# Performance work log

Measured on AMD Instinct MI355X. Metric: run time of the kernel, lower is better.

The kernel has to match this reference:

```python
import jax, jax.numpy as jnp
import numpy as np

N = 50000      # nodes
E = 1600000    # edges (avg degree 32)
IN = 128       # input feature dim
H = 4          # heads
C = 16         # out channels per head
NEG_SLOPE = 0.2


def setup_inputs() -> dict:
    key = jax.random.key(0)
    k = jax.random.split(key, 6)
    x = jax.random.normal(k[0], (N, IN), jnp.float32)
    edge_index = jax.random.randint(k[1], (2, E), 0, N, dtype=jnp.int32).astype(jnp.int64)
    W = jax.random.normal(k[2], (H * C, IN), jnp.float32) * (1.0 / np.sqrt(IN))
    att_src = jax.random.normal(k[3], (H, C), jnp.float32) * 0.1
    att_dst = jax.random.normal(k[4], (H, C), jnp.float32) * 0.1
    bias = jax.random.normal(k[5], (H * C,), jnp.float32) * 0.01
    return {"x": x, "edge_index": edge_index, "W": W,
            "att_src": att_src, "att_dst": att_dst, "bias": bias}


def reference(x, edge_index, W, att_src, att_dst, bias):
    # shared linear projection (PyG GATConv lin, no bias): [N, H, C]
    xp = (x @ W.T).reshape(-1, H, C)
    # per-node attention logits: [N, H]
    a_src = jnp.einsum('nhc,hc->nh', xp, att_src)
    a_dst = jnp.einsum('nhc,hc->nh', xp, att_dst)
    src, dst = edge_index[0], edge_index[1]  # messages flow src(j) -> dst(i)
    # per-edge scores: [E, H]
    e = jax.nn.leaky_relu(a_src[src] + a_dst[dst], negative_slope=NEG_SLOPE)
    # segment softmax over destination neighborhoods
    m = jax.ops.segment_max(e, dst, num_segments=N)           # [N, H]
    m = jnp.where(jnp.isfinite(m), m, 0.0)                     # empty segments
    ex = jnp.exp(e - m[dst])
    s = jax.ops.segment_sum(ex, dst, num_segments=N)           # [N, H]
    alpha = ex / (s[dst] + 1e-16)                              # [E, H]
    # weighted messages, scatter-add to destinations
    msg = (alpha[:, :, None] * xp[src]).reshape(E, H * C)      # [E, H*C]
    out = jax.ops.segment_sum(msg, dst, num_segments=N)        # [N, H*C]
    return out + bias
```

## Files before the change

### kernel.cpp

```cpp
#include <hip/hip_runtime.h>
#include <hip/hip_bf16.h>
#include <math.h>

#define N_NODES 50000
#define N_EDGES 1600000
#define IN_DIM  128
#define HC      64
#define NH      4
#define SLOTS   72
#define BSHIFT  6
#define BNODES  64
#define NB      782
#define BCAP    2432
#define BIN_BLOCKS 250
#define BIN_G   1600
#define GEMM_BLOCKS 391
#define GEMM_LDS 33792

__global__ __launch_bounds__(512) void bin_count_kernel(
    const int* __restrict__ ei, int* __restrict__ counts) {
    __shared__ int lcount[NB];
    int tid = (int)threadIdx.x;
    int bx  = (int)blockIdx.x;
    for (int j = tid; j < NB; j += 512) lcount[j] = 0;
    __syncthreads();
    const int4* dp = (const int4*)(ei + N_EDGES);
    int g0 = bx * BIN_G;
#pragma unroll
    for (int it = 0; it < 4; ++it) {
        int gi = it * 512 + tid;
        if (gi < BIN_G) {
            int4 dv = dp[g0 + gi];
            atomicAdd(&lcount[dv.x >> BSHIFT], 1);
            atomicAdd(&lcount[dv.y >> BSHIFT], 1);
            atomicAdd(&lcount[dv.z >> BSHIFT], 1);
            atomicAdd(&lcount[dv.w >> BSHIFT], 1);
        }
    }
    __syncthreads();
    for (int j = tid; j < NB; j += 512)
        counts[bx * NB + j] = lcount[j];
}

__global__ __launch_bounds__(256) void bin_scan_kernel(
    const int* __restrict__ counts, int* __restrict__ base,
    int* __restrict__ btot) {
    __shared__ int sc[256];
    int j = (int)blockIdx.x, t = (int)threadIdx.x;
    int v = (t < BIN_BLOCKS) ? counts[t * NB + j] : 0;
    sc[t] = v;
    __syncthreads();
#pragma unroll
    for (int off = 1; off < 256; off <<= 1) {
        int u = (t >= off) ? sc[t - off] : 0;
        __syncthreads();
        sc[t] += u;
        __syncthreads();
    }
    if (t < BIN_BLOCKS) base[t * NB + j] = sc[t] - v;
    if (t == BIN_BLOCKS - 1) btot[j] = sc[t];
}

__global__ __launch_bounds__(512) void bin_append_kernel(
    const int* __restrict__ ei, const int* __restrict__ base,
    unsigned int* __restrict__ barr) {
    __shared__ int lbase[NB], lcnt[NB];
    int tid = (int)threadIdx.x;
    int bx  = (int)blockIdx.x;
    for (int j = tid; j < NB; j += 512) {
        lbase[j] = base[bx * NB + j];
        lcnt[j]  = 0;
    }
    __syncthreads();
    const int4* sp = (const int4*)ei;
    const int4* dp = (const int4*)(ei + N_EDGES);
    int g0 = bx * BIN_G;
#pragma unroll
    for (int it = 0; it < 4; ++it) {
        int gi = it * 512 + tid;
        if (gi < BIN_G) {
            int4 sv = sp[g0 + gi];
            int4 dv = dp[g0 + gi];
            int s[4] = {sv.x, sv.y, sv.z, sv.w};
            int d[4] = {dv.x, dv.y, dv.z, dv.w};
#pragma unroll
            for (int u = 0; u < 4; ++u) {
                int bk = d[u] >> BSHIFT;
                int lp = atomicAdd(&lcnt[bk], 1);
                int pos = lbase[bk] + lp;
                if (pos < BCAP)
                    barr[(size_t)bk * BCAP + pos] =
                        (unsigned)s[u] | ((unsigned)(d[u] & (BNODES - 1)) << 20);
            }
        }
    }
}

__global__ __launch_bounds__(512) void gemm_kernel(
    const float* __restrict__ x, const float* __restrict__ W,
    const float* __restrict__ att_src, const float* __restrict__ att_dst,
    __hip_bfloat16* __restrict__ xp, float* __restrict__ a_src,
    float* __restrict__ a_dst) {
    extern __shared__ char smraw[];
    int tid = (int)threadIdx.x;
    int gb  = (int)blockIdx.x;
    float* Wl = (float*)smraw;
    const float4* W4 = (const float4*)W;
#pragma unroll
    for (int j = 0; j < 4; ++j) {
        int f = j * 512 + tid;
        int c = f >> 5, k4 = f & 31;
        *(float4*)&Wl[c * 132 + k4 * 4] = W4[f];
    }
    __syncthreads();

    int l = tid & 63, w = tid >> 6, q = l >> 4, i = l & 15;
    int n0 = gb * 128 + w * 16 + q * 4;
    int nj[4];
#pragma unroll
    for (int j = 0; j < 4; ++j) {
        int n = n0 + j;
        nj[j] = (n < N_NODES) ? n : N_NODES - 1;
    }
    const float* wlp = Wl + i * 132;
    float4 acc[4] = {{0,0,0,0},{0,0,0,0},{0,0,0,0},{0,0,0,0}};
    float4 xr[4], xn[4];
#pragma unroll
    for (int j = 0; j < 4; ++j) xr[j] = *(const float4*)(x + (size_t)nj[j] * IN_DIM);
#pragma unroll 2
    for (int k0 = 0; k0 < IN_DIM; k0 += 4) {
        if (k0 + 4 < IN_DIM) {
#pragma unroll
            for (int j = 0; j < 4; ++j)
                xn[j] = *(const float4*)(x + (size_t)nj[j] * IN_DIM + k0 + 4);
        }
        float4 wl0 = *(const float4*)(wlp + 0 * 16 * 132 + k0);
        float4 wl1 = *(const float4*)(wlp + 1 * 16 * 132 + k0);
        float4 wl2 = *(const float4*)(wlp + 2 * 16 * 132 + k0);
        float4 wl3 = *(const float4*)(wlp + 3 * 16 * 132 + k0);
#pragma unroll
        for (int j = 0; j < 4; ++j) {
            float4 xv = xr[j];
            acc[j].x = fmaf(xv.x, wl0.x, fmaf(xv.y, wl0.y, fmaf(xv.z, wl0.z, fmaf(xv.w, wl0.w, acc[j].x))));
            acc[j].y = fmaf(xv.x, wl1.x, fmaf(xv.y, wl1.y, fmaf(xv.z, wl1.z, fmaf(xv.w, wl1.w, acc[j].y))));
            acc[j].z = fmaf(xv.x, wl2.x, fmaf(xv.y, wl2.y, fmaf(xv.z, wl2.z, fmaf(xv.w, wl2.w, acc[j].z))));
            acc[j].w = fmaf(xv.x, wl3.x, fmaf(xv.y, wl3.y, fmaf(xv.z, wl3.z, fmaf(xv.w, wl3.w, acc[j].w))));
        }
#pragma unroll
        for (int j = 0; j < 4; ++j) xr[j] = xn[j];
    }

    float a_s0 = att_src[i], a_s1 = att_src[16 + i], a_s2 = att_src[32 + i], a_s3 = att_src[48 + i];
    float a_d0 = att_dst[i], a_d1 = att_dst[16 + i], a_d2 = att_dst[32 + i], a_d3 = att_dst[48 + i];
#pragma unroll
    for (int j = 0; j < 4; ++j) {
        int n = n0 + j;
        if (n < N_NODES) {
            __hip_bfloat16* xw = xp + (size_t)n * HC;
            xw[i]      = __float2bfloat16(acc[j].x);
            xw[16 + i] = __float2bfloat16(acc[j].y);
            xw[32 + i] = __float2bfloat16(acc[j].z);
            xw[48 + i] = __float2bfloat16(acc[j].w);
            float4 ps, pd;
            ps.x = acc[j].x * a_s0; ps.y = acc[j].y * a_s1;
            ps.z = acc[j].z * a_s2; ps.w = acc[j].w * a_s3;
            pd.x = acc[j].x * a_d0; pd.y = acc[j].y * a_d1;
            pd.z = acc[j].z * a_d2; pd.w = acc[j].w * a_d3;
#pragma unroll
            for (int off = 1; off < 16; off <<= 1) {
                ps.x += __shfl_xor(ps.x, off, 64); ps.y += __shfl_xor(ps.y, off, 64);
                ps.z += __shfl_xor(ps.z, off, 64); ps.w += __shfl_xor(ps.w, off, 64);
                pd.x += __shfl_xor(pd.x, off, 64); pd.y += __shfl_xor(pd.y, off, 64);
                pd.z += __shfl_xor(pd.z, off, 64); pd.w += __shfl_xor(pd.w, off, 64);
            }
            if (i == 0) {
                *(float4*)(a_src + n * NH) = ps;
                *(float4*)(a_dst + n * NH) = pd;
            }
        }
    }
}

__global__ __launch_bounds__(512) void fused_gather_kernel(
    const unsigned int* __restrict__ barr, const int* __restrict__ btot,
    const float* __restrict__ a_src, const float* __restrict__ a_dst,
    const __hip_bfloat16* __restrict__ xp, const float* __restrict__ bias,
    float* __restrict__ out) {
    __shared__ int lcsr[BNODES * SLOTS];
    __shared__ int deg[BNODES];
    int b = blockIdx.x, tid = (int)threadIdx.x;
    if (tid < BNODES) deg[tid] = 0;
    __syncthreads();
    int n = btot[b];
    n = (n < BCAP) ? n : BCAP;
    const unsigned int* src = barr + (size_t)b * BCAP;

    for (int i0 = 0; i0 < n; i0 += 2048) {
        int ibase = i0 + tid * 4;
        unsigned v[4]; bool val[4]; int dp[4], pos[4];
        if (ibase < n) {
            uint4 r = *(const uint4*)(src + ibase);
            v[0] = r.x; v[1] = r.y; v[2] = r.z; v[3] = r.w;
        } else { v[0] = v[1] = v[2] = v[3] = 0u; }
#pragma unroll
        for (int u = 0; u < 4; ++u) {
            val[u] = (ibase + u) < n;
            dp[u] = (int)(v[u] >> 20);
            if (val[u]) pos[u] = atomicAdd(&deg[dp[u]], 1);
        }
#pragma unroll
        for (int u = 0; u < 4; ++u)
            if (val[u] && pos[u] < SLOTS)
                lcsr[dp[u] * SLOTS + pos[u]] = (int)(v[u] & 0xFFFFF);
    }
    __syncthreads();

    int l = tid & 63;
    int w = tid >> 6;
    int g = l >> 3;
    int i = l & 7;
    int h = i >> 1;
    int dl = w * 8 + g;
    int dst = (b << BSHIFT) + dl;
    int dg = deg[dl];
    dg = (dg < SLOTS) ? dg : SLOTS;
    int dstc = (dst < N_NODES) ? dst : 0;
    float adh = a_dst[dstc * NH + h];

    int sreg[9];
#pragma unroll
    for (int k = 0; k < 9; ++k) sreg[k] = lcsr[dl * SLOTS + k * 8 + i];

    const unsigned short* xpi = (const unsigned short*)xp + 8 * i;
    const float* asrch = a_src + h;
    int gsel = l & 56;
    float a0=0,a1=0,a2=0,a3=0,a4=0,a5=0,a6=0,a7=0;
    float dsum = 0.f;

#pragma unroll
    for (int k = 0; k < 9; ++k) {
        if (dg > k * 8) {
            int cnt = dg - k * 8;
            int reg = sreg[k];
            int s8[8]; float g8[8]; uint4 t8[8];
#pragma unroll
            for (int u = 0; u < 8; ++u) {
                int raw = __shfl(reg, gsel | u, 64);
                s8[u] = (u < cnt) ? raw : 0;
            }
#pragma unroll
            for (int u = 0; u < 8; ++u) g8[u] = asrch[s8[u] * NH];
#pragma unroll
            for (int u = 0; u < 8; ++u)
                t8[u] = *(const uint4*)(xpi + (size_t)s8[u] * HC);
#pragma unroll
            for (int u = 0; u < 8; ++u) {
                float e = g8[u] + adh;
                e = fmaxf(e, 0.2f * e);
                float wv = (u < cnt) ? __expf(e) : 0.f;
                dsum += wv;
                uint4 t = t8[u];
                a0 = fmaf(wv, __uint_as_float(t.x << 16),          a0);
                a1 = fmaf(wv, __uint_as_float(t.x & 0xffff0000u),  a1);
                a2 = fmaf(wv, __uint_as_float(t.y << 16),          a2);
                a3 = fmaf(wv, __uint_as_float(t.y & 0xffff0000u),  a3);
                a4 = fmaf(wv, __uint_as_float(t.z << 16),          a4);
                a5 = fmaf(wv, __uint_as_float(t.z & 0xffff0000u),  a5);
                a6 = fmaf(wv, __uint_as_float(t.w << 16),          a6);
                a7 = fmaf(wv, __uint_as_float(t.w & 0xffff0000u),  a7);
            }
        }
    }
    if (dst < N_NODES) {
        float inv = 1.f / (dsum + 1e-16f);
        float4 b0 = *(const float4*)(bias + 8 * i);
        float4 b1 = *(const float4*)(bias + 8 * i + 4);
        float4 o0, o1;
        o0.x = a0 * inv + b0.x; o0.y = a1 * inv + b0.y;
        o0.z = a2 * inv + b0.z; o0.w = a3 * inv + b0.w;
        o1.x = a4 * inv + b1.x; o1.y = a5 * inv + b1.y;
        o1.z = a6 * inv + b1.z; o1.w = a7 * inv + b1.w;
        float* op = out + (size_t)dst * HC + 8 * i;
        *(float4*)op = o0;
        *(float4*)(op + 4) = o1;
    }
}

extern "C" void kernel_launch(void* const* d_in, const int* in_sizes, int n_in,
                              void* d_out, int out_size, void* d_ws, size_t ws_size,
                              hipStream_t stream) {
    const float* x       = (const float*)d_in[0];
    const int*   ei      = (const int*)d_in[1];
    const float* W       = (const float*)d_in[2];
    const float* att_src = (const float*)d_in[3];
    const float* att_dst = (const float*)d_in[4];
    const float* bias    = (const float*)d_in[5];
    float* out = (float*)d_out;

    char* ws = (char*)d_ws;
    __hip_bfloat16* xp      = (__hip_bfloat16*)(ws);
    float*          a_srcv  = (float*)(ws + 6400000);
    float*          a_dstv  = (float*)(ws + 7200000);
    int*            btot    = (int*)  (ws + 8000000);
    unsigned int*   barr    = (unsigned int*)(ws + 8016384);
    int*            counts  = (int*)  (ws + 15624192);
    int*            basem   = (int*)  (ws + 16406272);

    bin_count_kernel<<<BIN_BLOCKS, 512, 0, stream>>>(ei, counts);
    bin_scan_kernel<<<NB, 256, 0, stream>>>(counts, basem, btot);
    bin_append_kernel<<<BIN_BLOCKS, 512, 0, stream>>>(ei, basem, barr);
    gemm_kernel<<<GEMM_BLOCKS, 512, GEMM_LDS, stream>>>(
        x, W, att_src, att_dst, xp, a_srcv, a_dstv);
    fused_gather_kernel<<<NB, 512, 0, stream>>>(barr, btot,
                                                a_srcv, a_dstv, xp, bias, out);
}
```

Baseline: 153.2 us.

## Fuse GEMM with bin counting, split bins finer, prefetch next gather group

Merges the projection GEMM and the edge bin-count pass into one launch. Extra blocks do the per-block destination histogram, so counting runs alongside the GEMM and one kernel launch disappears. Doubles the number of binning blocks (halving edges per block) and widens the scan to 512 threads to match. In the gather kernel, the shuffle of the next group's source indices and its a_src loads are issued before the current group's exp/FMA work, hiding that latency. The cost is more partial-count rows to scan and higher register pressure in the gather loop.

```diff
diff --git a/kernel.cpp b/kernel.cpp
--- a/kernel.cpp
+++ b/kernel.cpp
@@ -12,98 +12,47 @@
 #define BNODES  64
 #define NB      782
 #define BCAP    2432
-#define BIN_BLOCKS 250
-#define BIN_G   1600
+#define BIN_BLOCKS 500
+#define BIN_G   800
 #define GEMM_BLOCKS 391
+#define FAT_GRID (GEMM_BLOCKS + BIN_BLOCKS)
 #define GEMM_LDS 33792
 
-__global__ __launch_bounds__(512) void bin_count_kernel(
-    const int* __restrict__ ei, int* __restrict__ counts) {
-    __shared__ int lcount[NB];
+__global__ __launch_bounds__(512) void gemm_count_kernel(
+    const float* __restrict__ x, const float* __restrict__ W,
+    const float* __restrict__ att_src, const float* __restrict__ att_dst,
+    const int* __restrict__ ei,
+    __hip_bfloat16* __restrict__ xp, float* __restrict__ a_src,
+    float* __restrict__ a_dst, int* __restrict__ counts) {
+    extern __shared__ char smraw[];
     int tid = (int)threadIdx.x;
     int bx  = (int)blockIdx.x;
-    for (int j = tid; j < NB; j += 512) lcount[j] = 0;
-    __syncthreads();
-    const int4* dp = (const int4*)(ei + N_EDGES);
-    int g0 = bx * BIN_G;
-#pragma unroll
-    for (int it = 0; it < 4; ++it) {
-        int gi = it * 512 + tid;
-        if (gi < BIN_G) {
-            int4 dv = dp[g0 + gi];
-            atomicAdd(&lcount[dv.x >> BSHIFT], 1);
-            atomicAdd(&lcount[dv.y >> BSHIFT], 1);
-            atomicAdd(&lcount[dv.z >> BSHIFT], 1);
-            atomicAdd(&lcount[dv.w >> BSHIFT], 1);
-        }
-    }
-    __syncthreads();
-    for (int j = tid; j < NB; j += 512)
-        counts[bx * NB + j] = lcount[j];
-}
-
-__global__ __launch_bounds__(256) void bin_scan_kernel(
-    const int* __restrict__ counts, int* __restrict__ base,
-    int* __restrict__ btot) {
-    __shared__ int sc[256];
-    int j = (int)blockIdx.x, t = (int)threadIdx.x;
-    int v = (t < BIN_BLOCKS) ? counts[t * NB + j] : 0;
-    sc[t] = v;
-    __syncthreads();
-#pragma unroll
-    for (int off = 1; off < 256; off <<= 1) {
-        int u = (t >= off) ? sc[t - off] : 0;
+
+    if (bx >= GEMM_BLOCKS) {
+        int cb = bx - GEMM_BLOCKS;
+        int* lcount = (int*)smraw;
+        for (int j = tid; j < NB; j += 512) lcount[j] = 0;
         __syncthreads();
-        sc[t] += u;
+        const int4* dp = (const int4*)(ei + N_EDGES);
+        int g0 = cb * BIN_G;
+#pragma unroll
+        for (int it = 0; it < 2; ++it) {
+            int gi = it * 512 + tid;
+            if (gi < BIN_G) {
+                int4 dv = dp[g0 + gi];
+                atomicAdd(&lcount[dv.x >> BSHIFT], 1);
+                atomicAdd(&lcount[dv.y >> BSHIFT], 1);
+                atomicAdd(&lcount[dv.z >> BSHIFT], 1);
+                atomicAdd(&lcount[dv.w >> BSHIFT], 1);
+            }
+        }
         __syncthreads();
-    }
-    if (t < BIN_BLOCKS) base[t * NB + j] = sc[t] - v;
-    if (t == BIN_BLOCKS - 1) btot[j] = sc[t];
-}
-
-__global__ __launch_bounds__(512) void bin_append_kernel(
-    const int* __restrict__ ei, const int* __restrict__ base,
-    unsigned int* __restrict__ barr) {
-    __shared__ int lbase[NB], lcnt[NB];
-    int tid = (int)threadIdx.x;
-    int bx  = (int)blockIdx.x;
-    for (int j = tid; j < NB; j += 512) {
-        lbase[j] = base[bx * NB + j];
-        lcnt[j]  = 0;
-    }
-    __syncthreads();
-    const int4* sp = (const int4*)ei;
-    const int4* dp = (const int4*)(ei + N_EDGES);
-    int g0 = bx * BIN_G;
-#pragma unroll
-    for (int it = 0; it < 4; ++it) {
-        int gi = it * 512 + tid;
-        if (gi < BIN_G) {
-            int4 sv = sp[g0 + gi];
-            int4 dv = dp[g0 + gi];
-            int s[4] = {sv.x, sv.y, sv.z, sv.w};
-            int d[4] = {dv.x, dv.y, dv.z, dv.w};
-#pragma unroll
-            for (int u = 0; u < 4; ++u) {
-                int bk = d[u] >> BSHIFT;
-                int lp = atomicAdd(&lcnt[bk], 1);
-                int pos = lbase[bk] + lp;
-                if (pos < BCAP)
-                    barr[(size_t)bk * BCAP + pos] =
-                        (unsigned)s[u] | ((unsigned)(d[u] & (BNODES - 1)) << 20);
-            }
-        }
-    }
-}
-
-__global__ __launch_bounds__(512) void gemm_kernel(
-    const float* __restrict__ x, const float* __restrict__ W,
-    const float* __restrict__ att_src, const float* __restrict__ att_dst,
-    __hip_bfloat16* __restrict__ xp, float* __restrict__ a_src,
-    float* __restrict__ a_dst) {
-    extern __shared__ char smraw[];
-    int tid = (int)threadIdx.x;
-    int gb  = (int)blockIdx.x;
+        for (int j = tid; j < NB; j += 512)
+            counts[cb * NB + j] = lcount[j];
+        return;
+    }
+
+    int gb = bx;
     float* Wl = (float*)smraw;
     const float4* W4 = (const float4*)W;
 #pragma unroll
@@ -181,6 +130,60 @@
     }
 }
 
+__global__ __launch_bounds__(512) void bin_scan_kernel(
+    const int* __restrict__ counts, int* __restrict__ base,
+    int* __restrict__ btot) {
+    __shared__ int sc[512];
+    int j = (int)blockIdx.x, t = (int)threadIdx.x;
+    int v = (t < BIN_BLOCKS) ? counts[t * NB + j] : 0;
+    sc[t] = v;
+    __syncthreads();
+#pragma unroll
+    for (int off = 1; off < 512; off <<= 1) {
+        int u = (t >= off) ? sc[t - off] : 0;
+        __syncthreads();
+        sc[t] += u;
+        __syncthreads();
+    }
+    if (t < BIN_BLOCKS) base[t * NB + j] = sc[t] - v;
+    if (t == BIN_BLOCKS - 1) btot[j] = sc[t];
+}
+
+__global__ __launch_bounds__(512) void bin_append_kernel(
+    const int* __restrict__ ei, const int* __restrict__ base,
+    unsigned int* __restrict__ barr) {
+    __shared__ int lbase[NB], lcnt[NB];
+    int tid = (int)threadIdx.x;
+    int bx  = (int)blockIdx.x;
+    for (int j = tid; j < NB; j += 512) {
+        lbase[j] = base[bx * NB + j];
+        lcnt[j]  = 0;
+    }
+    __syncthreads();
+    const int4* sp = (const int4*)ei;
+    const int4* dp = (const int4*)(ei + N_EDGES);
+    int g0 = bx * BIN_G;
+#pragma unroll
+    for (int it = 0; it < 2; ++it) {
+        int gi = it * 512 + tid;
+        if (gi < BIN_G) {
+            int4 sv = sp[g0 + gi];
+            int4 dv = dp[g0 + gi];
+            int s[4] = {sv.x, sv.y, sv.z, sv.w};
+            int d[4] = {dv.x, dv.y, dv.z, dv.w};
+#pragma unroll
+            for (int u = 0; u < 4; ++u) {
+                int bk = d[u] >> BSHIFT;
+                int lp = atomicAdd(&lcnt[bk], 1);
+                int pos = lbase[bk] + lp;
+                if (pos < BCAP)
+                    barr[(size_t)bk * BCAP + pos] =
+                        (unsigned)s[u] | ((unsigned)(d[u] & (BNODES - 1)) << 20);
+            }
+        }
+    }
+}
+
 __global__ __launch_bounds__(512) void fused_gather_kernel(
     const unsigned int* __restrict__ barr, const int* __restrict__ btot,
     const float* __restrict__ a_src, const float* __restrict__ a_dst,
@@ -237,25 +240,41 @@
     float a0=0,a1=0,a2=0,a3=0,a4=0,a5=0,a6=0,a7=0;
     float dsum = 0.f;
 
+    int s8a[8]; float g8a[8];
+    if (dg > 0) {
+        int cnt0 = dg;
+#pragma unroll
+        for (int u = 0; u < 8; ++u) {
+            int raw = __shfl(sreg[0], gsel | u, 64);
+            s8a[u] = (u < cnt0) ? raw : 0;
+        }
+#pragma unroll
+        for (int u = 0; u < 8; ++u) g8a[u] = asrch[s8a[u] * NH];
+    }
+
 #pragma unroll
     for (int k = 0; k < 9; ++k) {
         if (dg > k * 8) {
             int cnt = dg - k * 8;
-            int reg = sreg[k];
-            int s8[8]; float g8[8]; uint4 t8[8];
+            uint4 t8[8];
+#pragma unroll
+            for (int u = 0; u < 8; ++u)
+                t8[u] = *(const uint4*)(xpi + (size_t)s8a[u] * HC);
+            int s8n[8]; float g8n[8];
+            bool nx = (k + 1 < 9) && (dg > (k + 1) * 8);
+            if (nx) {
+                int cntn = dg - (k + 1) * 8;
+#pragma unroll
+                for (int u = 0; u < 8; ++u) {
+                    int raw = __shfl(sreg[k + 1], gsel | u, 64);
+                    s8n[u] = (u < cntn) ? raw : 0;
+                }
+#pragma unroll
+                for (int u = 0; u < 8; ++u) g8n[u] = asrch[s8n[u] * NH];
+            }
 #pragma unroll
             for (int u = 0; u < 8; ++u) {
-                int raw = __shfl(reg, gsel | u, 64);
-                s8[u] = (u < cnt) ? raw : 0;
-            }
-#pragma unroll
-            for (int u = 0; u < 8; ++u) g8[u] = asrch[s8[u] * NH];
-#pragma unroll
-            for (int u = 0; u < 8; ++u)
-                t8[u] = *(const uint4*)(xpi + (size_t)s8[u] * HC);
-#pragma unroll
-            for (int u = 0; u < 8; ++u) {
-                float e = g8[u] + adh;
+                float e = g8a[u] + adh;
                 e = fmaxf(e, 0.2f * e);
                 float wv = (u < cnt) ? __expf(e) : 0.f;
                 dsum += wv;
@@ -269,6 +288,10 @@
                 a6 = fmaf(wv, __uint_as_float(t.w << 16),          a6);
                 a7 = fmaf(wv, __uint_as_float(t.w & 0xffff0000u),  a7);
             }
+            if (nx) {
+#pragma unroll
+                for (int u = 0; u < 8; ++u) { s8a[u] = s8n[u]; g8a[u] = g8n[u]; }
+            }
         }
     }
     if (dst < N_NODES) {
@@ -303,14 +326,13 @@
     float*          a_dstv  = (float*)(ws + 7200000);
     int*            btot    = (int*)  (ws + 8000000);
     unsigned int*   barr    = (unsigned int*)(ws + 8016384);
-    int*            counts  = (int*)  (ws + 15624192);
-    int*            basem   = (int*)  (ws + 16406272);
-
-    bin_count_kernel<<<BIN_BLOCKS, 512, 0, stream>>>(ei, counts);
-    bin_scan_kernel<<<NB, 256, 0, stream>>>(counts, basem, btot);
+    int*            counts  = (int*)  (ws + 15700000);
+    int*            basem   = (int*)  (ws + 17300000);
+
+    gemm_count_kernel<<<FAT_GRID, 512, GEMM_LDS, stream>>>(
+        x, W, att_src, att_dst, ei, xp, a_srcv, a_dstv, counts);
+    bin_scan_kernel<<<NB, 512, 0, stream>>>(counts, basem, btot);
     bin_append_kernel<<<BIN_BLOCKS, 512, 0, stream>>>(ei, basem, barr);
-    gemm_kernel<<<GEMM_BLOCKS, 512, GEMM_LDS, stream>>>(
-        x, W, att_src, att_dst, xp, a_srcv, a_dstv);
     fused_gather_kernel<<<NB, 512, 0, stream>>>(barr, btot,
                                                 a_srcv, a_dstv, xp, bias, out);
 }
```

Measured after the change: 161.9 us. 5.6% more time.
